# Optimization experiments

Measured on AMD Instinct MI355X. Metric: run time of the kernel, lower is better.

Reference implementation:

```python
import jax, jax.numpy as jnp
import numpy as np

COS_EPS = 1e-8  # torch F.cosine_similarity eps


def setup_inputs() -> dict:
    key = jax.random.key(0)
    k1, k2 = jax.random.split(key)
    x = jax.random.normal(k1, (8192, 512), dtype=jnp.float32)
    class_logits = jax.random.normal(k2, (8192, 100), dtype=jnp.float32)
    return {"x": x, "class_logits": class_logits}


def reference(x, class_logits):
    N, D = x.shape
    C = class_logits.shape[1]

    # class_logits.clone().detach()
    logits = jax.lax.stop_gradient(class_logits)
    pred = jax.nn.softmax(logits, axis=1)
    max_logit = pred.max(axis=1)          # [N]
    max_cls = pred.argmax(axis=1)         # [N] int

    # graph(): pairwise cosine similarity = normalize rows + gram matmul
    norms = jnp.linalg.norm(x, axis=1, keepdims=True)
    xn = x / jnp.maximum(norms, COS_EPS)
    mat = xn @ xn.T                       # [N, N]

    x_agg = mat @ x + x                   # [N, D]
    x_new = jax.lax.stop_gradient(x_agg)

    # update_prototype: per-class weighted scatter-add then mean over counts
    weighted = x_new * max_logit[:, None]                     # [N, D]
    sums = jax.ops.segment_sum(weighted, max_cls, num_segments=C)      # [C, D]
    counts = jax.ops.segment_sum(jnp.ones((N,), x.dtype), max_cls, num_segments=C)  # [C]
    prototypes = jnp.where(counts[:, None] > 0,
                           sums / jnp.maximum(counts, 1.0)[:, None],
                           jnp.zeros_like(sums))              # [C, D]

    # inter_class_matrix[i, j] = prototypes[j] - prototypes[i]
    inter_class_matrix = prototypes[None, :, :] - prototypes[:, None, :]  # [C, C, D]
    return prototypes, inter_class_matrix
```

## Files before the change

kernel.cpp:

```cpp
#include <hip/hip_runtime.h>
#include <math.h>

#define N_ROWS 8192
#define D_DIM  512
#define C_CLS  100

typedef unsigned short u16;
typedef unsigned int u32;
typedef __attribute__((ext_vector_type(8))) _Float16 half8;
typedef __attribute__((ext_vector_type(4))) float floatx4;

#define WS_G      0
#define WS_GP     262144
#define WS_INV    5505024
#define WS_WV     5513216
#define WS_CLS    5521408
#define WS_CNT    5529600
#define WS_U      5538048
#define WS_V      5589248
#define WS_ZTH    5640448

#define LDA 517

typedef const __attribute__((address_space(1))) u32* gp32;
typedef __attribute__((address_space(3))) u32* lp32;
__device__ __forceinline__ void cp16(const u16* g, u16* l) {
    __builtin_amdgcn_global_load_lds((gp32)g, (lp32)l, 16, 0, 0);
}

__device__ __forceinline__ u16 f2h(float v) {
    _Float16 h = (_Float16)v;
    return *(u16*)&h;
}

__global__ __launch_bounds__(256) void kA(const float* __restrict__ logits,
        const float* __restrict__ x, float* __restrict__ wv, int* __restrict__ cls,
        float* __restrict__ inv, u16* __restrict__ zth, int* __restrict__ cnt) {
    __shared__ float xs[16 * LDA];
    __shared__ float ns[4][16];
    __shared__ float sv_s[16];
    int bx = blockIdx.x, t = threadIdx.x;
    if (bx < 1024) {
        int lane = t & 63;
        int row0 = (bx << 3) + ((t >> 6) << 1);
        #pragma unroll
        for (int rr = 0; rr < 2; ++rr) {
            int row = row0 + rr;
            const float* lrow = logits + (size_t)row * C_CLS;
            float v1 = lrow[lane];
            bool has2 = (lane + 64) < C_CLS;
            float v2 = has2 ? lrow[lane + 64] : -INFINITY;
            float m; int idx;
            if (v2 > v1) { m = v2; idx = lane + 64; } else { m = v1; idx = lane; }
            #pragma unroll
            for (int off = 32; off >= 1; off >>= 1) {
                float om = __shfl_down(m, off);
                int   oi = __shfl_down(idx, off);
                if (om > m || (om == m && oi < idx)) { m = om; idx = oi; }
            }
            m = __shfl(m, 0);
            idx = __shfl(idx, 0);
            float s = expf(v1 - m) + (has2 ? expf(v2 - m) : 0.0f);
            #pragma unroll
            for (int off = 32; off >= 1; off >>= 1) s += __shfl_down(s, off);
            if (lane == 0) {
                wv[row] = 1.0f / s;
                cls[row] = idx;
                atomicAdd(&cnt[idx], 1);
            }
        }
        return;
    }
    int r0 = (bx - 1024) << 4;
    const float* src = x + (size_t)r0 * D_DIM;
    #pragma unroll
    for (int i = 0; i < 8; ++i) {
        int e = i * 1024 + t * 4;
        int r = e >> 9, c = e & 511;
        *(float4*)&xs[r * LDA + c] = *(const float4*)&src[e];
    }
    __syncthreads();
    {
        int r = t & 15, seg = t >> 4;
        const float* row = &xs[r * LDA + seg * 32];
        float ss = 0.f;
        #pragma unroll
        for (int jj = 0; jj < 32; ++jj) { float v = row[jj]; ss += v * v; }
        ns[0][r] = 0.f;
        __syncthreads();
        atomicAdd(&ns[0][r], ss);
    }
    __syncthreads();
    if (t < 16) {
        float iv = 1.0f / fmaxf(sqrtf(ns[0][t]), 1e-8f);
        inv[r0 + t] = iv;
        sv_s[t] = sqrtf(iv);
    }
    __syncthreads();
    int c = t >> 1, rq = (t & 1) * 8;
    float svl[8];
    #pragma unroll
    for (int ii = 0; ii < 8; ++ii) svl[ii] = sv_s[rq + ii];
    #pragma unroll
    for (int ct = 0; ct < 4; ++ct) {
        int d = ct * 128 + c;
        u16 o[8];
        #pragma unroll
        for (int ii = 0; ii < 8; ++ii)
            o[ii] = f2h(xs[(rq + ii) * LDA + d] * svl[ii]);
        uint4 val = make_uint4((u32)o[0] | ((u32)o[1] << 16),
                               (u32)o[2] | ((u32)o[3] << 16),
                               (u32)o[4] | ((u32)o[5] << 16),
                               (u32)o[6] | ((u32)o[7] << 16));
        *(uint4*)&zth[(size_t)d * N_ROWS + r0 + rq] = val;
    }
}

__global__ __launch_bounds__(256) void kC(const u16* __restrict__ zth,
        const float* __restrict__ x, const float* __restrict__ inv,
        const float* __restrict__ wv, const int* __restrict__ cls,
        float* __restrict__ Gp, float* __restrict__ u_arr, float* __restrict__ v_arr) {
    __shared__ __attribute__((aligned(16))) union {
        struct { u16 Ah[2][128 * 32], Bh[2][128 * 32]; } g;
        struct { float us[4][64], vs[4][64]; } uv;
    } sm;
    int bx = blockIdx.x, t = threadIdx.x;
    if (bx >= 80) {
        int idx = bx - 80;
        int c = idx >> 3, jc = idx & 7;
        int g = t >> 6, lane = t & 63;
        int j = jc * 64 + lane;
        float ua = 0.f, va = 0.f;
        int base = g * 2048;
        for (int b = 0; b < 2048; b += 64) {
            int mb = base + b;
            unsigned long long mask = __ballot(cls[mb + lane] == c);
            while (mask) {
                int bit = __builtin_ctzll(mask);
                mask &= mask - 1;
                int m = mb + bit;
                float wm = wv[m];
                float wi = wm * inv[m];
                float xv = x[(size_t)m * D_DIM + j];
                ua += wi * xv; va += wm * xv;
            }
        }
        sm.uv.us[g][lane] = ua; sm.uv.vs[g][lane] = va;
        __syncthreads();
        if (g == 0) {
            u_arr[(size_t)c * D_DIM + j] = sm.uv.us[0][lane] + sm.uv.us[1][lane] + sm.uv.us[2][lane] + sm.uv.us[3][lane];
            v_arr[(size_t)c * D_DIM + j] = sm.uv.vs[0][lane] + sm.uv.vs[1][lane] + sm.uv.vs[2][lane] + sm.uv.vs[3][lane];
        }
        return;
    }
    int tile = bx % 10;
    int p = bx / 10;
    int ti = tile < 4 ? 0 : (tile < 7 ? 1 : (tile < 9 ? 2 : 3));
    int tj = tile - (ti == 0 ? 0 : (ti == 1 ? 3 : (ti == 2 ? 5 : 6)));
    int i0 = ti << 7, j0 = tj << 7;
    bool diag = (ti == tj);
    int kb = p << 10;
    int w = t >> 6, l = t & 63;
    int srow = t >> 2, slot = t & 3;
    int xslot = slot ^ ((srow >> 1) & 3);
    int lm = l & 15, lg = l >> 4;
    int rs = (lm >> 1) & 3;
    floatx4 acc[4][4];
    #pragma unroll
    for (int mi = 0; mi < 4; ++mi)
        #pragma unroll
        for (int ni = 0; ni < 4; ++ni) acc[mi][ni] = (floatx4){0.f, 0.f, 0.f, 0.f};
    int d0 = srow * 32 + slot * 8;
    int d1 = (64 + srow) * 32 + slot * 8;
    const size_t ga0 = (size_t)(i0 + srow) * N_ROWS + kb + (xslot << 3);
    const size_t ga1 = (size_t)(i0 + 64 + srow) * N_ROWS + kb + (xslot << 3);
    const size_t gb0 = (size_t)(j0 + srow) * N_ROWS + kb + (xslot << 3);
    const size_t gb1 = (size_t)(j0 + 64 + srow) * N_ROWS + kb + (xslot << 3);
    cp16(zth + ga0, sm.g.Ah[0] + d0);
    cp16(zth + ga1, sm.g.Ah[0] + d1);
    if (!diag) {
        cp16(zth + gb0, sm.g.Bh[0] + d0);
        cp16(zth + gb1, sm.g.Bh[0] + d1);
    }
    __syncthreads();
    for (int s = 0; s < 32; ++s) {
        int cur = s & 1, nxt = cur ^ 1;
        if (s + 1 < 32) {
            int ks = (s + 1) << 5;
            cp16(zth + ga0 + ks, sm.g.Ah[nxt] + d0);
            cp16(zth + ga1 + ks, sm.g.Ah[nxt] + d1);
            if (!diag) {
                cp16(zth + gb0 + ks, sm.g.Bh[nxt] + d0);
                cp16(zth + gb1 + ks, sm.g.Bh[nxt] + d1);
            }
        }
        const u16* Bhs = diag ? sm.g.Ah[cur] : sm.g.Bh[cur];
        half8 ah[4], bh[4];
        #pragma unroll
        for (int mi = 0; mi < 4; ++mi) {
            int off = (((w & 1) << 6) + (mi << 4) + lm) * 32 + ((lg ^ rs) << 3);
            ah[mi] = *(const half8*)&sm.g.Ah[cur][off];
        }
        #pragma unroll
        for (int ni = 0; ni < 4; ++ni) {
            int off = (((w >> 1) << 6) + (ni << 4) + lm) * 32 + ((lg ^ rs) << 3);
            bh[ni] = *(const half8*)&Bhs[off];
        }
        #pragma unroll
        for (int mi = 0; mi < 4; ++mi)
            #pragma unroll
            for (int ni = 0; ni < 4; ++ni)
                acc[mi][ni] = __builtin_amdgcn_mfma_f32_16x16x32_f16(ah[mi], bh[ni], acc[mi][ni], 0, 0, 0);
        __syncthreads();
    }
    float* Gb = Gp + ((size_t)(p * 10 + tile) << 14);
    #pragma unroll
    for (int mi = 0; mi < 4; ++mi) {
        int row0 = ((w & 1) << 6) + (mi << 4) + (lg << 2);
        #pragma unroll
        for (int ni = 0; ni < 4; ++ni) {
            int col = ((w >> 1) << 6) + (ni << 4) + lm;
            #pragma unroll
            for (int r = 0; r < 4; ++r)
                Gb[(size_t)(row0 + r) * 128 + col] = acc[mi][ni][r];
        }
    }
}

__global__ __launch_bounds__(256) void kR(const float* __restrict__ Gp,
                                          float* __restrict__ G) {
    int i = blockIdx.x * 256 + threadIdx.x;
    int r = i >> 9, c = i & 511;
    int tr = r >> 7, tc = c >> 7, rr = r & 127, cc = c & 127;
    if (tr > tc) { int tmp = tr; tr = tc; tc = tmp; tmp = rr; rr = cc; cc = tmp; }
    int tid = tr * 4 + tc - ((tr * (tr + 1)) >> 1);
    const float* src = Gp + ((size_t)tid << 14) + rr * 128 + cc;
    float s = 0.f;
    #pragma unroll
    for (int p = 0; p < 8; ++p) s += src[(size_t)p * 163840];
    G[i] = s;
}

__global__ __launch_bounds__(256) void kD(const float* __restrict__ u_arr,
        const float* __restrict__ v_arr, const int* __restrict__ cnt,
        const float* __restrict__ G, float* __restrict__ out) {
    __shared__ float us[8][512];
    int g = blockIdx.x >> 4;
    int panel = blockIdx.x & 15;
    int t = threadIdx.x;
    for (int idx = t; idx < 8 * 512; idx += 256) {
        int ci = idx >> 9, k = idx & 511;
        int cc = g * 8 + ci;
        us[ci][k] = (cc < C_CLS) ? u_arr[(size_t)cc * D_DIM + k] : 0.f;
    }
    __syncthreads();
    int ci = t >> 5, cj = t & 31;
    int c = g * 8 + ci;
    int j = panel * 32 + cj;
    float acc = 0.f;
    #pragma unroll 8
    for (int k = 0; k < D_DIM; ++k)
        acc += us[ci][k] * G[(size_t)k * D_DIM + j];
    if (c < C_CLS) {
        int n = cnt[c];
        float s = (n > 0) ? 1.0f / (float)n : 0.0f;
        out[(size_t)c * D_DIM + j] = (v_arr[(size_t)c * D_DIM + j] + acc) * s;
    }
}

__global__ __launch_bounds__(256) void kE(const float* __restrict__ proto,
                                          float* __restrict__ inter) {
    int pair = blockIdx.x * 4 + (threadIdx.x >> 6);
    int i = pair / C_CLS;
    int j = pair - i * C_CLS;
    int d = (threadIdx.x & 63) << 3;
    float4 pj0 = *(const float4*)&proto[j * D_DIM + d];
    float4 pj1 = *(const float4*)&proto[j * D_DIM + d + 4];
    float4 pi0 = *(const float4*)&proto[i * D_DIM + d];
    float4 pi1 = *(const float4*)&proto[i * D_DIM + d + 4];
    float4 r0, r1;
    r0.x = pj0.x - pi0.x; r0.y = pj0.y - pi0.y; r0.z = pj0.z - pi0.z; r0.w = pj0.w - pi0.w;
    r1.x = pj1.x - pi1.x; r1.y = pj1.y - pi1.y; r1.z = pj1.z - pi1.z; r1.w = pj1.w - pi1.w;
    *(float4*)&inter[(size_t)pair * D_DIM + d]     = r0;
    *(float4*)&inter[(size_t)pair * D_DIM + d + 4] = r1;
}

extern "C" void kernel_launch(void* const* d_in, const int* in_sizes, int n_in,
                              void* d_out, int out_size, void* d_ws, size_t ws_size,
                              hipStream_t stream) {
    const float* x      = (const float*)d_in[0];
    const float* logits = (const float*)d_in[1];
    float* out = (float*)d_out;
    float* ws  = (float*)d_ws;
    float* G     = ws + WS_G;
    float* Gp    = ws + WS_GP;
    float* inv   = ws + WS_INV;
    float* wv    = ws + WS_WV;
    int*   cls   = (int*)(ws + WS_CLS);
    int*   cnt   = (int*)(ws + WS_CNT);
    float* u_arr = ws + WS_U;
    float* v_arr = ws + WS_V;
    u16* zth = (u16*)(ws + WS_ZTH);

    hipMemsetAsync(cnt, 0, 128 * sizeof(int), stream);
    kA<<<1536, 256, 0, stream>>>(logits, x, wv, cls, inv, zth, cnt);
    kC<<<880, 256, 0, stream>>>(zth, x, inv, wv, cls, Gp, u_arr, v_arr);
    kR<<<1024, 256, 0, stream>>>(Gp, G);
    kD<<<208, 256, 0, stream>>>(u_arr, v_arr, cnt, G, out);
    kE<<<C_CLS * C_CLS / 4, 256, 0, stream>>>(out, out + C_CLS * D_DIM);
}
```

Measured before the change: 170.8 us.

## Fuse all stages into one cooperative persistent kernel with grid syncs

Result: slower. 309.4 us (+81.1%).

```diff
diff --git a/kernel.cpp b/kernel.cpp
--- a/kernel.cpp
+++ b/kernel.cpp
@@ -1,9 +1,13 @@
 #include <hip/hip_runtime.h>
+#include <hip/hip_cooperative_groups.h>
 #include <math.h>
+
+namespace cg = cooperative_groups;
 
 #define N_ROWS 8192
 #define D_DIM  512
 #define C_CLS  100
+#define SPLITK 16
 
 typedef unsigned short u16;
 typedef unsigned int u32;
@@ -33,11 +37,264 @@
     return *(u16*)&h;
 }
 
+__global__ __launch_bounds__(256, 3) void kFused(
+        const float* __restrict__ logits, const float* __restrict__ x,
+        float* __restrict__ wv, int* __restrict__ cls, float* __restrict__ inv,
+        u16* __restrict__ zth, int* __restrict__ cnt, float* __restrict__ Gp,
+        float* __restrict__ G, float* __restrict__ u_arr, float* __restrict__ v_arr,
+        float* __restrict__ out) {
+    __shared__ __attribute__((aligned(16))) union {
+        struct { float xs[16 * LDA]; float ns[16]; float sv[16]; } p1;
+        struct { u16 Ah[2][128 * 32], Bh[2][128 * 32]; } g;
+        struct { float us[4][64], vs[4][64]; } uvs;
+        struct { float us[8][512]; } d;
+    } sm;
+    cg::grid_group grid = cg::this_grid();
+    int bx = blockIdx.x, t = threadIdx.x, gdim = gridDim.x;
+    int lane = t & 63, wid = t >> 6;
+
+    if (bx == 0 && t < 128) cnt[t] = 0;
+    for (int u = bx; u < 512; u += gdim) {
+        __syncthreads();
+        int r0 = u << 4;
+        #pragma unroll
+        for (int rr = 0; rr < 4; ++rr) {
+            int row = r0 + (wid << 2) + rr;
+            const float* lrow = logits + (size_t)row * C_CLS;
+            float v1 = lrow[lane];
+            bool has2 = (lane + 64) < C_CLS;
+            float v2 = has2 ? lrow[lane + 64] : -INFINITY;
+            float m; int idx;
+            if (v2 > v1) { m = v2; idx = lane + 64; } else { m = v1; idx = lane; }
+            #pragma unroll
+            for (int off = 32; off >= 1; off >>= 1) {
+                float om = __shfl_down(m, off);
+                int   oi = __shfl_down(idx, off);
+                if (om > m || (om == m && oi < idx)) { m = om; idx = oi; }
+            }
+            m = __shfl(m, 0); idx = __shfl(idx, 0);
+            float s = expf(v1 - m) + (has2 ? expf(v2 - m) : 0.0f);
+            #pragma unroll
+            for (int off = 32; off >= 1; off >>= 1) s += __shfl_down(s, off);
+            if (lane == 0) { wv[row] = 1.0f / s; cls[row] = idx; }
+        }
+        const float* src = x + (size_t)r0 * D_DIM;
+        #pragma unroll
+        for (int i = 0; i < 8; ++i) {
+            int e = i * 1024 + t * 4;
+            int r = e >> 9, c = e & 511;
+            *(float4*)&sm.p1.xs[r * LDA + c] = *(const float4*)&src[e];
+        }
+        __syncthreads();
+        {
+            int r = t & 15, seg = t >> 4;
+            const float* row = &sm.p1.xs[r * LDA + seg * 32];
+            float ss = 0.f;
+            #pragma unroll
+            for (int jj = 0; jj < 32; ++jj) { float v = row[jj]; ss += v * v; }
+            sm.p1.ns[r] = 0.f;
+            __syncthreads();
+            atomicAdd(&sm.p1.ns[r], ss);
+        }
+        __syncthreads();
+        if (t < 16) {
+            float iv = 1.0f / fmaxf(sqrtf(sm.p1.ns[t]), 1e-8f);
+            inv[r0 + t] = iv;
+            sm.p1.sv[t] = sqrtf(iv);
+        }
+        __syncthreads();
+        int c = t >> 1, rq = (t & 1) * 8;
+        float svl[8];
+        #pragma unroll
+        for (int ii = 0; ii < 8; ++ii) svl[ii] = sm.p1.sv[rq + ii];
+        #pragma unroll
+        for (int ct = 0; ct < 4; ++ct) {
+            int d = ct * 128 + c;
+            u16 o[8];
+            #pragma unroll
+            for (int ii = 0; ii < 8; ++ii)
+                o[ii] = f2h(sm.p1.xs[(rq + ii) * LDA + d] * svl[ii]);
+            uint4 val = make_uint4((u32)o[0] | ((u32)o[1] << 16),
+                                   (u32)o[2] | ((u32)o[3] << 16),
+                                   (u32)o[4] | ((u32)o[5] << 16),
+                                   (u32)o[6] | ((u32)o[7] << 16));
+            *(uint4*)&zth[(size_t)d * N_ROWS + r0 + rq] = val;
+        }
+    }
+    grid.sync();
+
+    for (int u = bx; u < 160 + 800; u += gdim) {
+        __syncthreads();
+        if (u >= 160) {
+            int idx = u - 160;
+            int c = idx >> 3, jc = idx & 7;
+            int g = wid;
+            int j = jc * 64 + lane;
+            float ua = 0.f, va = 0.f;
+            int base = g * 2048;
+            for (int b = 0; b < 2048; b += 64) {
+                int mb = base + b;
+                unsigned long long mask = __ballot(cls[mb + lane] == c);
+                while (mask) {
+                    int bit = __builtin_ctzll(mask);
+                    mask &= mask - 1;
+                    int m = mb + bit;
+                    float wm = wv[m];
+                    float wi = wm * inv[m];
+                    float xv = x[(size_t)m * D_DIM + j];
+                    ua += wi * xv; va += wm * xv;
+                }
+            }
+            sm.uvs.us[g][lane] = ua; sm.uvs.vs[g][lane] = va;
+            __syncthreads();
+            if (g == 0) {
+                u_arr[(size_t)c * D_DIM + j] = sm.uvs.us[0][lane] + sm.uvs.us[1][lane] + sm.uvs.us[2][lane] + sm.uvs.us[3][lane];
+                v_arr[(size_t)c * D_DIM + j] = sm.uvs.vs[0][lane] + sm.uvs.vs[1][lane] + sm.uvs.vs[2][lane] + sm.uvs.vs[3][lane];
+            }
+        } else {
+            int tile = u % 10;
+            int p = u / 10;
+            int ti = tile < 4 ? 0 : (tile < 7 ? 1 : (tile < 9 ? 2 : 3));
+            int tj = tile - (ti == 0 ? 0 : (ti == 1 ? 3 : (ti == 2 ? 5 : 6)));
+            int i0 = ti << 7, j0 = tj << 7;
+            bool diag = (ti == tj);
+            int kb = p << 9;
+            int w = wid, l = lane;
+            int srow = t >> 2, slot = t & 3;
+            int xslot = slot ^ ((srow >> 1) & 3);
+            int lm = l & 15, lg = l >> 4;
+            int rs = (lm >> 1) & 3;
+            floatx4 acc[4][4];
+            #pragma unroll
+            for (int mi = 0; mi < 4; ++mi)
+                #pragma unroll
+                for (int ni = 0; ni < 4; ++ni) acc[mi][ni] = (floatx4){0.f, 0.f, 0.f, 0.f};
+            int d0 = srow * 32 + slot * 8;
+            int d1 = (64 + srow) * 32 + slot * 8;
+            const size_t ga0 = (size_t)(i0 + srow) * N_ROWS + kb + (xslot << 3);
+            const size_t ga1 = (size_t)(i0 + 64 + srow) * N_ROWS + kb + (xslot << 3);
+            const size_t gb0 = (size_t)(j0 + srow) * N_ROWS + kb + (xslot << 3);
+            const size_t gb1 = (size_t)(j0 + 64 + srow) * N_ROWS + kb + (xslot << 3);
+            cp16(zth + ga0, sm.g.Ah[0] + d0);
+            cp16(zth + ga1, sm.g.Ah[0] + d1);
+            if (!diag) {
+                cp16(zth + gb0, sm.g.Bh[0] + d0);
+                cp16(zth + gb1, sm.g.Bh[0] + d1);
+            }
+            __syncthreads();
+            for (int s = 0; s < 16; ++s) {
+                int cur = s & 1, nxt = cur ^ 1;
+                if (s + 1 < 16) {
+                    int ks = (s + 1) << 5;
+                    cp16(zth + ga0 + ks, sm.g.Ah[nxt] + d0);
+                    cp16(zth + ga1 + ks, sm.g.Ah[nxt] + d1);
+                    if (!diag) {
+                        cp16(zth + gb0 + ks, sm.g.Bh[nxt] + d0);
+                        cp16(zth + gb1 + ks, sm.g.Bh[nxt] + d1);
+                    }
+                }
+                const u16* Bhs = diag ? sm.g.Ah[cur] : sm.g.Bh[cur];
+                half8 ah[4], bh[4];
+                #pragma unroll
+                for (int mi = 0; mi < 4; ++mi) {
+                    int off = (((w & 1) << 6) + (mi << 4) + lm) * 32 + ((lg ^ rs) << 3);
+                    ah[mi] = *(const half8*)&sm.g.Ah[cur][off];
+                }
+                #pragma unroll
+                for (int ni = 0; ni < 4; ++ni) {
+                    int off = (((w >> 1) << 6) + (ni << 4) + lm) * 32 + ((lg ^ rs) << 3);
+                    bh[ni] = *(const half8*)&Bhs[off];
+                }
+                #pragma unroll
+                for (int mi = 0; mi < 4; ++mi)
+                    #pragma unroll
+                    for (int ni = 0; ni < 4; ++ni)
+                        acc[mi][ni] = __builtin_amdgcn_mfma_f32_16x16x32_f16(ah[mi], bh[ni], acc[mi][ni], 0, 0, 0);
+                __syncthreads();
+            }
+            float* Gb = Gp + ((size_t)u << 14);
+            #pragma unroll
+            for (int mi = 0; mi < 4; ++mi) {
+                int row0 = ((w & 1) << 6) + (mi << 4) + (lg << 2);
+                #pragma unroll
+                for (int ni = 0; ni < 4; ++ni) {
+                    int col = ((w >> 1) << 6) + (ni << 4) + lm;
+                    #pragma unroll
+                    for (int r = 0; r < 4; ++r)
+                        Gb[(size_t)(row0 + r) * 128 + col] = acc[mi][ni][r];
+                }
+            }
+        }
+    }
+    grid.sync();
+
+    {
+        int nth = gdim << 8;
+        for (int i = (bx << 8) + t; i < D_DIM * D_DIM; i += nth) {
+            int r = i >> 9, c = i & 511;
+            int tr = r >> 7, tc = c >> 7, rr = r & 127, cc = c & 127;
+            if (tr > tc) { int tmp = tr; tr = tc; tc = tmp; tmp = rr; rr = cc; cc = tmp; }
+            int tid = tr * 4 + tc - ((tr * (tr + 1)) >> 1);
+            const float* src = Gp + ((size_t)tid << 14) + rr * 128 + cc;
+            float s = 0.f;
+            #pragma unroll
+            for (int p = 0; p < SPLITK; ++p) s += src[(size_t)p * 163840];
+            G[i] = s;
+        }
+        if (bx < 64 && t < 128)
+            atomicAdd(&cnt[cls[(bx << 7) + t]], 1);
+    }
+    grid.sync();
+
+    for (int u = bx; u < 208; u += gdim) {
+        __syncthreads();
+        int g = u >> 4, panel = u & 15;
+        for (int idx = t; idx < 8 * 512; idx += 256) {
+            int ci = idx >> 9, k = idx & 511;
+            int cc = g * 8 + ci;
+            sm.d.us[ci][k] = (cc < C_CLS) ? u_arr[(size_t)cc * D_DIM + k] : 0.f;
+        }
+        __syncthreads();
+        int ci = t >> 5, cj = t & 31;
+        int c = g * 8 + ci;
+        int j = panel * 32 + cj;
+        float acc = 0.f;
+        #pragma unroll 8
+        for (int k = 0; k < D_DIM; ++k)
+            acc += sm.d.us[ci][k] * G[(size_t)k * D_DIM + j];
+        if (c < C_CLS) {
+            int n = cnt[c];
+            float s = (n > 0) ? 1.0f / (float)n : 0.0f;
+            out[(size_t)c * D_DIM + j] = (v_arr[(size_t)c * D_DIM + j] + acc) * s;
+        }
+    }
+    grid.sync();
+
+    {
+        float* inter = out + C_CLS * D_DIM;
+        for (int u = bx; u < (C_CLS * C_CLS) / 4; u += gdim) {
+            int pair = (u << 2) + wid;
+            int i = pair / C_CLS;
+            int j = pair - i * C_CLS;
+            int d = lane << 3;
+            float4 pj0 = *(const float4*)&out[j * D_DIM + d];
+            float4 pj1 = *(const float4*)&out[j * D_DIM + d + 4];
+            float4 pi0 = *(const float4*)&out[i * D_DIM + d];
+            float4 pi1 = *(const float4*)&out[i * D_DIM + d + 4];
+            float4 r0, r1;
+            r0.x = pj0.x - pi0.x; r0.y = pj0.y - pi0.y; r0.z = pj0.z - pi0.z; r0.w = pj0.w - pi0.w;
+            r1.x = pj1.x - pi1.x; r1.y = pj1.y - pi1.y; r1.z = pj1.z - pi1.z; r1.w = pj1.w - pi1.w;
+            *(float4*)&inter[(size_t)pair * D_DIM + d]     = r0;
+            *(float4*)&inter[(size_t)pair * D_DIM + d + 4] = r1;
+        }
+    }
+}
+
 __global__ __launch_bounds__(256) void kA(const float* __restrict__ logits,
         const float* __restrict__ x, float* __restrict__ wv, int* __restrict__ cls,
         float* __restrict__ inv, u16* __restrict__ zth, int* __restrict__ cnt) {
     __shared__ float xs[16 * LDA];
-    __shared__ float ns[4][16];
+    __shared__ float ns[16];
     __shared__ float sv_s[16];
     int bx = blockIdx.x, t = threadIdx.x;
     if (bx < 1024) {
@@ -58,16 +315,11 @@
                 int   oi = __shfl_down(idx, off);
                 if (om > m || (om == m && oi < idx)) { m = om; idx = oi; }
             }
-            m = __shfl(m, 0);
-            idx = __shfl(idx, 0);
+            m = __shfl(m, 0); idx = __shfl(idx, 0);
             float s = expf(v1 - m) + (has2 ? expf(v2 - m) : 0.0f);
             #pragma unroll
             for (int off = 32; off >= 1; off >>= 1) s += __shfl_down(s, off);
-            if (lane == 0) {
-                wv[row] = 1.0f / s;
-                cls[row] = idx;
-                atomicAdd(&cnt[idx], 1);
-            }
+            if (lane == 0) { wv[row] = 1.0f / s; cls[row] = idx; atomicAdd(&cnt[idx], 1); }
         }
         return;
     }
@@ -86,13 +338,13 @@
         float ss = 0.f;
         #pragma unroll
         for (int jj = 0; jj < 32; ++jj) { float v = row[jj]; ss += v * v; }
-        ns[0][r] = 0.f;
-        __syncthreads();
-        atomicAdd(&ns[0][r], ss);
+        ns[r] = 0.f;
+        __syncthreads();
+        atomicAdd(&ns[r], ss);
     }
     __syncthreads();
     if (t < 16) {
-        float iv = 1.0f / fmaxf(sqrtf(ns[0][t]), 1e-8f);
+        float iv = 1.0f / fmaxf(sqrtf(ns[t]), 1e-8f);
         inv[r0 + t] = iv;
         sv_s[t] = sqrtf(iv);
     }
@@ -125,8 +377,8 @@
         struct { float us[4][64], vs[4][64]; } uv;
     } sm;
     int bx = blockIdx.x, t = threadIdx.x;
-    if (bx >= 80) {
-        int idx = bx - 80;
+    if (bx >= 160) {
+        int idx = bx - 160;
         int c = idx >> 3, jc = idx & 7;
         int g = t >> 6, lane = t & 63;
         int j = jc * 64 + lane;
@@ -159,7 +411,7 @@
     int tj = tile - (ti == 0 ? 0 : (ti == 1 ? 3 : (ti == 2 ? 5 : 6)));
     int i0 = ti << 7, j0 = tj << 7;
     bool diag = (ti == tj);
-    int kb = p << 10;
+    int kb = p << 9;
     int w = t >> 6, l = t & 63;
     int srow = t >> 2, slot = t & 3;
     int xslot = slot ^ ((srow >> 1) & 3);
@@ -178,21 +430,15 @@
     const size_t gb1 = (size_t)(j0 + 64 + srow) * N_ROWS + kb + (xslot << 3);
     cp16(zth + ga0, sm.g.Ah[0] + d0);
     cp16(zth + ga1, sm.g.Ah[0] + d1);
-    if (!diag) {
-        cp16(zth + gb0, sm.g.Bh[0] + d0);
-        cp16(zth + gb1, sm.g.Bh[0] + d1);
-    }
+    if (!diag) { cp16(zth + gb0, sm.g.Bh[0] + d0); cp16(zth + gb1, sm.g.Bh[0] + d1); }
     __syncthreads();
-    for (int s = 0; s < 32; ++s) {
+    for (int s = 0; s < 16; ++s) {
         int cur = s & 1, nxt = cur ^ 1;
-        if (s + 1 < 32) {
+        if (s + 1 < 16) {
             int ks = (s + 1) << 5;
             cp16(zth + ga0 + ks, sm.g.Ah[nxt] + d0);
             cp16(zth + ga1 + ks, sm.g.Ah[nxt] + d1);
-            if (!diag) {
-                cp16(zth + gb0 + ks, sm.g.Bh[nxt] + d0);
-                cp16(zth + gb1 + ks, sm.g.Bh[nxt] + d1);
-            }
+            if (!diag) { cp16(zth + gb0 + ks, sm.g.Bh[nxt] + d0); cp16(zth + gb1 + ks, sm.g.Bh[nxt] + d1); }
         }
         const u16* Bhs = diag ? sm.g.Ah[cur] : sm.g.Bh[cur];
         half8 ah[4], bh[4];
@@ -213,7 +459,7 @@
                 acc[mi][ni] = __builtin_amdgcn_mfma_f32_16x16x32_f16(ah[mi], bh[ni], acc[mi][ni], 0, 0, 0);
         __syncthreads();
     }
-    float* Gb = Gp + ((size_t)(p * 10 + tile) << 14);
+    float* Gb = Gp + ((size_t)bx << 14);
     #pragma unroll
     for (int mi = 0; mi < 4; ++mi) {
         int row0 = ((w & 1) << 6) + (mi << 4) + (lg << 2);
@@ -237,7 +483,7 @@
     const float* src = Gp + ((size_t)tid << 14) + rr * 128 + cc;
     float s = 0.f;
     #pragma unroll
-    for (int p = 0; p < 8; ++p) s += src[(size_t)p * 163840];
+    for (int p = 0; p < SPLITK; ++p) s += src[(size_t)p * 163840];
     G[i] = s;
 }
 
@@ -302,9 +548,29 @@
     float* v_arr = ws + WS_V;
     u16* zth = (u16*)(ws + WS_ZTH);
 
+    static int nblk = 0;
+    static int coop_ok = 1;
+    if (nblk == 0) {
+        int bpc = 0;
+        hipError_t e = hipOccupancyMaxActiveBlocksPerMultiprocessor(&bpc, kFused, 256, 0);
+        if (e != hipSuccess || bpc < 1) { coop_ok = 0; bpc = 1; }
+        if (bpc > 8) bpc = 8;
+        nblk = bpc * 256;
+    }
+
+    if (coop_ok) {
+        void* args[] = { (void*)&logits, (void*)&x, (void*)&wv, (void*)&cls,
+                         (void*)&inv, (void*)&zth, (void*)&cnt, (void*)&Gp,
+                         (void*)&G, (void*)&u_arr, (void*)&v_arr, (void*)&out };
+        hipError_t e = hipLaunchCooperativeKernel((const void*)kFused, dim3(nblk),
+                                                  dim3(256), args, 0, stream);
+        if (e == hipSuccess) return;
+        coop_ok = 0;
+    }
+
     hipMemsetAsync(cnt, 0, 128 * sizeof(int), stream);
     kA<<<1536, 256, 0, stream>>>(logits, x, wv, cls, inv, zth, cnt);
-    kC<<<880, 256, 0, stream>>>(zth, x, inv, wv, cls, Gp, u_arr, v_arr);
+    kC<<<960, 256, 0, stream>>>(zth, x, inv, wv, cls, Gp, u_arr, v_arr);
     kR<<<1024, 256, 0, stream>>>(Gp, G);
     kD<<<208, 256, 0, stream>>>(u_arr, v_arr, cnt, G, out);
     kE<<<C_CLS * C_CLS / 4, 256, 0, stream>>>(out, out + C_CLS * D_DIM);
```

## Quadruple split-K for Gram kernel, restructure transpose, and fold class counts into kC

Applied to the files above, without the earlier changes.

Result: slower. 179.3 us (+5.0%).

```diff
diff --git a/kernel.cpp b/kernel.cpp
--- a/kernel.cpp
+++ b/kernel.cpp
@@ -4,6 +4,7 @@
 #define N_ROWS 8192
 #define D_DIM  512
 #define C_CLS  100
+#define SPLITK 32
 
 typedef unsigned short u16;
 typedef unsigned int u32;
@@ -20,8 +21,6 @@
 #define WS_V      5589248
 #define WS_ZTH    5640448
 
-#define LDA 517
-
 typedef const __attribute__((address_space(1))) u32* gp32;
 typedef __attribute__((address_space(3))) u32* lp32;
 __device__ __forceinline__ void cp16(const u16* g, u16* l) {
@@ -35,14 +34,13 @@
 
 __global__ __launch_bounds__(256) void kA(const float* __restrict__ logits,
         const float* __restrict__ x, float* __restrict__ wv, int* __restrict__ cls,
-        float* __restrict__ inv, u16* __restrict__ zth, int* __restrict__ cnt) {
-    __shared__ float xs[16 * LDA];
-    __shared__ float ns[4][16];
-    __shared__ float sv_s[16];
+        float* __restrict__ inv, u16* __restrict__ zth) {
+    __shared__ float xs[64 * 132];
+    __shared__ float sv_s[64];
     int bx = blockIdx.x, t = threadIdx.x;
+    int lane = t & 63, w = t >> 6;
     if (bx < 1024) {
-        int lane = t & 63;
-        int row0 = (bx << 3) + ((t >> 6) << 1);
+        int row0 = (bx << 3) + (w << 1);
         #pragma unroll
         for (int rr = 0; rr < 2; ++rr) {
             int row = row0 + rr;
@@ -58,83 +56,83 @@
                 int   oi = __shfl_down(idx, off);
                 if (om > m || (om == m && oi < idx)) { m = om; idx = oi; }
             }
-            m = __shfl(m, 0);
-            idx = __shfl(idx, 0);
+            m = __shfl(m, 0); idx = __shfl(idx, 0);
             float s = expf(v1 - m) + (has2 ? expf(v2 - m) : 0.0f);
             #pragma unroll
             for (int off = 32; off >= 1; off >>= 1) s += __shfl_down(s, off);
-            if (lane == 0) {
-                wv[row] = 1.0f / s;
-                cls[row] = idx;
-                atomicAdd(&cnt[idx], 1);
+            if (lane == 0) { wv[row] = 1.0f / s; cls[row] = idx; }
+        }
+        return;
+    }
+    int r0 = (bx - 1024) << 6;
+    for (int rr = 0; rr < 16; ++rr) {
+        int rl = (w << 4) + rr;
+        const float* row = x + (size_t)(r0 + rl) * D_DIM + (lane << 3);
+        float4 a = *(const float4*)row;
+        float4 b = *(const float4*)(row + 4);
+        float ss = a.x * a.x + a.y * a.y + a.z * a.z + a.w * a.w
+                 + b.x * b.x + b.y * b.y + b.z * b.z + b.w * b.w;
+        #pragma unroll
+        for (int off = 32; off >= 1; off >>= 1) ss += __shfl_down(ss, off);
+        if (lane == 0) {
+            float iv = 1.0f / fmaxf(sqrtf(ss), 1e-8f);
+            inv[r0 + rl] = iv;
+            sv_s[rl] = sqrtf(iv);
+        }
+    }
+    __syncthreads();
+    for (int it = 0; it < 4; ++it) {
+        int dB = it << 7;
+        #pragma unroll
+        for (int i = 0; i < 8; ++i) {
+            int e = (i << 10) + (t << 2);
+            int m = e >> 7, dl = e & 127;
+            *(float4*)&xs[m * 132 + dl] =
+                *(const float4*)&x[(size_t)(r0 + m) * D_DIM + dB + dl];
+        }
+        __syncthreads();
+        int dp = t >> 1, h = t & 1;
+        u16* dst = zth + (size_t)(dB + dp) * N_ROWS + r0 + (h << 5);
+        #pragma unroll
+        for (int q = 0; q < 4; ++q) {
+            u16 o[8];
+            #pragma unroll
+            for (int ii = 0; ii < 8; ++ii) {
+                int m = (h << 5) + (q << 3) + ii;
+                o[ii] = f2h(xs[m * 132 + dp] * sv_s[m]);
             }
-        }
-        return;
-    }
-    int r0 = (bx - 1024) << 4;
-    const float* src = x + (size_t)r0 * D_DIM;
-    #pragma unroll
-    for (int i = 0; i < 8; ++i) {
-        int e = i * 1024 + t * 4;
-        int r = e >> 9, c = e & 511;
-        *(float4*)&xs[r * LDA + c] = *(const float4*)&src[e];
-    }
-    __syncthreads();
-    {
-        int r = t & 15, seg = t >> 4;
-        const float* row = &xs[r * LDA + seg * 32];
-        float ss = 0.f;
-        #pragma unroll
-        for (int jj = 0; jj < 32; ++jj) { float v = row[jj]; ss += v * v; }
-        ns[0][r] = 0.f;
+            uint4 val = make_uint4((u32)o[0] | ((u32)o[1] << 16),
+                                   (u32)o[2] | ((u32)o[3] << 16),
+                                   (u32)o[4] | ((u32)o[5] << 16),
+                                   (u32)o[6] | ((u32)o[7] << 16));
+            *(uint4*)&dst[q << 3] = val;
+        }
         __syncthreads();
-        atomicAdd(&ns[0][r], ss);
-    }
-    __syncthreads();
-    if (t < 16) {
-        float iv = 1.0f / fmaxf(sqrtf(ns[0][t]), 1e-8f);
-        inv[r0 + t] = iv;
-        sv_s[t] = sqrtf(iv);
-    }
-    __syncthreads();
-    int c = t >> 1, rq = (t & 1) * 8;
-    float svl[8];
-    #pragma unroll
-    for (int ii = 0; ii < 8; ++ii) svl[ii] = sv_s[rq + ii];
-    #pragma unroll
-    for (int ct = 0; ct < 4; ++ct) {
-        int d = ct * 128 + c;
-        u16 o[8];
-        #pragma unroll
-        for (int ii = 0; ii < 8; ++ii)
-            o[ii] = f2h(xs[(rq + ii) * LDA + d] * svl[ii]);
-        uint4 val = make_uint4((u32)o[0] | ((u32)o[1] << 16),
-                               (u32)o[2] | ((u32)o[3] << 16),
-                               (u32)o[4] | ((u32)o[5] << 16),
-                               (u32)o[6] | ((u32)o[7] << 16));
-        *(uint4*)&zth[(size_t)d * N_ROWS + r0 + rq] = val;
     }
 }
 
 __global__ __launch_bounds__(256) void kC(const u16* __restrict__ zth,
         const float* __restrict__ x, const float* __restrict__ inv,
         const float* __restrict__ wv, const int* __restrict__ cls,
-        float* __restrict__ Gp, float* __restrict__ u_arr, float* __restrict__ v_arr) {
+        float* __restrict__ Gp, float* __restrict__ u_arr, float* __restrict__ v_arr,
+        int* __restrict__ cnt) {
     __shared__ __attribute__((aligned(16))) union {
         struct { u16 Ah[2][128 * 32], Bh[2][128 * 32]; } g;
-        struct { float us[4][64], vs[4][64]; } uv;
+        struct { float us[4][64], vs[4][64]; int cnts[4]; } uv;
     } sm;
     int bx = blockIdx.x, t = threadIdx.x;
-    if (bx >= 80) {
-        int idx = bx - 80;
+    if (bx >= 320) {
+        int idx = bx - 320;
         int c = idx >> 3, jc = idx & 7;
         int g = t >> 6, lane = t & 63;
         int j = jc * 64 + lane;
         float ua = 0.f, va = 0.f;
+        int pc = 0;
         int base = g * 2048;
         for (int b = 0; b < 2048; b += 64) {
             int mb = base + b;
             unsigned long long mask = __ballot(cls[mb + lane] == c);
+            pc += __popcll(mask);
             while (mask) {
                 int bit = __builtin_ctzll(mask);
                 mask &= mask - 1;
@@ -146,10 +144,13 @@
             }
         }
         sm.uv.us[g][lane] = ua; sm.uv.vs[g][lane] = va;
+        if (lane == 0) sm.uv.cnts[g] = pc;
         __syncthreads();
         if (g == 0) {
             u_arr[(size_t)c * D_DIM + j] = sm.uv.us[0][lane] + sm.uv.us[1][lane] + sm.uv.us[2][lane] + sm.uv.us[3][lane];
             v_arr[(size_t)c * D_DIM + j] = sm.uv.vs[0][lane] + sm.uv.vs[1][lane] + sm.uv.vs[2][lane] + sm.uv.vs[3][lane];
+            if (lane == 0 && jc == 0)
+                cnt[c] = sm.uv.cnts[0] + sm.uv.cnts[1] + sm.uv.cnts[2] + sm.uv.cnts[3];
         }
         return;
     }
@@ -159,7 +160,7 @@
     int tj = tile - (ti == 0 ? 0 : (ti == 1 ? 3 : (ti == 2 ? 5 : 6)));
     int i0 = ti << 7, j0 = tj << 7;
     bool diag = (ti == tj);
-    int kb = p << 10;
+    int kb = p << 8;
     int w = t >> 6, l = t & 63;
     int srow = t >> 2, slot = t & 3;
     int xslot = slot ^ ((srow >> 1) & 3);
@@ -183,9 +184,9 @@
         cp16(zth + gb1, sm.g.Bh[0] + d1);
     }
     __syncthreads();
-    for (int s = 0; s < 32; ++s) {
+    for (int s = 0; s < 8; ++s) {
         int cur = s & 1, nxt = cur ^ 1;
-        if (s + 1 < 32) {
+        if (s + 1 < 8) {
             int ks = (s + 1) << 5;
             cp16(zth + ga0 + ks, sm.g.Ah[nxt] + d0);
             cp16(zth + ga1 + ks, sm.g.Ah[nxt] + d1);
@@ -213,7 +214,7 @@
                 acc[mi][ni] = __builtin_amdgcn_mfma_f32_16x16x32_f16(ah[mi], bh[ni], acc[mi][ni], 0, 0, 0);
         __syncthreads();
     }
-    float* Gb = Gp + ((size_t)(p * 10 + tile) << 14);
+    float* Gb = Gp + ((size_t)bx << 14);
     #pragma unroll
     for (int mi = 0; mi < 4; ++mi) {
         int row0 = ((w & 1) << 6) + (mi << 4) + (lg << 2);
@@ -237,7 +238,7 @@
     const float* src = Gp + ((size_t)tid << 14) + rr * 128 + cc;
     float s = 0.f;
     #pragma unroll
-    for (int p = 0; p < 8; ++p) s += src[(size_t)p * 163840];
+    for (int p = 0; p < SPLITK; ++p) s += src[(size_t)p * 163840];
     G[i] = s;
 }
 
@@ -302,9 +303,8 @@
     float* v_arr = ws + WS_V;
     u16* zth = (u16*)(ws + WS_ZTH);
 
-    hipMemsetAsync(cnt, 0, 128 * sizeof(int), stream);
-    kA<<<1536, 256, 0, stream>>>(logits, x, wv, cls, inv, zth, cnt);
-    kC<<<880, 256, 0, stream>>>(zth, x, inv, wv, cls, Gp, u_arr, v_arr);
+    kA<<<1152, 256, 0, stream>>>(logits, x, wv, cls, inv, zth);
+    kC<<<1120, 256, 0, stream>>>(zth, x, inv, wv, cls, Gp, u_arr, v_arr, cnt);
     kR<<<1024, 256, 0, stream>>>(Gp, G);
     kD<<<208, 256, 0, stream>>>(u_arr, v_arr, cnt, G, out);
     kE<<<C_CLS * C_CLS / 4, 256, 0, stream>>>(out, out + C_CLS * D_DIM);
```
